# Optimization experiments

Hardware: AMD Instinct MI355X
Metric: run time of the kernel (lower is better)

## Reference

```python
import jax, jax.numpy as jnp
import numpy as np

B, S, E, H = 2, 2048, 1024, 16
DH = E // H  # 64


def setup_inputs() -> dict:
    key = jax.random.key(0)
    ks = jax.random.split(key, 5)
    scale = 1.0 / np.sqrt(E)
    x = jax.random.normal(ks[0], (B, S, E), dtype=jnp.float32)
    # stacked per-head kqv Linear weights: out = x @ Wkqv[h] + bkqv[h], producing (k, q, v) chunks
    Wkqv = jax.random.normal(ks[1], (H, E, 3 * DH), dtype=jnp.float32) * scale
    bkqv = jax.random.normal(ks[2], (H, 3 * DH), dtype=jnp.float32) * scale
    Wo = jax.random.normal(ks[3], (E, E), dtype=jnp.float32) * scale
    bo = jax.random.normal(ks[4], (E,), dtype=jnp.float32) * scale
    return {"x": x, "Wkqv": Wkqv, "bkqv": bkqv, "Wo": Wo, "bo": bo}


def reference(x, Wkqv, bkqv, Wo, bo):
    b, s, e = x.shape
    h, _, f = Wkqv.shape
    dh = f // 3
    # per-head projection, fused over heads: [b, h, s, 3*dh]
    kqv = jnp.einsum('bse,hef->bhsf', x, Wkqv) + bkqv[None, :, None, :]
    # chunk order in the original is k, q, v
    k, q, v = jnp.split(kqv, 3, axis=-1)
    scores = jnp.einsum('bhqd,bhkd->bhqk', q, k) / jnp.sqrt(jnp.asarray(dh, x.dtype))
    causal = jnp.tril(jnp.ones((s, s), dtype=bool))  # slice of the tril buffer
    scores = jnp.where(causal[None, None], scores, -jnp.inf)
    weights = jax.nn.softmax(scores, axis=-1)
    sa = jnp.einsum('bhqk,bhkd->bhqd', weights, v)
    # concat heads along feature dim (head order preserved)
    sa = sa.transpose(0, 2, 1, 3).reshape(b, s, h * dh)
    return sa @ Wo + bo
```

## Files before the change

### kernel.cpp

```cpp
#include <hip/hip_runtime.h>
#include <hip/hip_bf16.h>

typedef __attribute__((ext_vector_type(8))) short bf16x8;
typedef __attribute__((ext_vector_type(4))) float f32x4;
typedef __attribute__((ext_vector_type(2))) unsigned u32x2;
typedef __attribute__((ext_vector_type(4))) unsigned u32x4;
typedef unsigned short u16;

#define NEG_INF (-__builtin_inff())

__device__ __forceinline__ void gload16(const void* g, void* l) {
  __builtin_amdgcn_global_load_lds(
      (const __attribute__((address_space(1))) void*)g,
      (__attribute__((address_space(3))) void*)l, 16, 0, 0);
}

__device__ __forceinline__ u16 f2b(float f) {
  union { float f; unsigned u; } v;
  v.f = f;
  unsigned r = v.u + 0x7fff + ((v.u >> 16) & 1);
  return (u16)(r >> 16);
}

__device__ __forceinline__ unsigned cvt_pk_bf16(float a, float b) {
  unsigned r;
  asm("v_cvt_pk_bf16_f32 %0, %1, %2" : "=v"(r) : "v"(a), "v"(b));
  return r;
}

__global__ __launch_bounds__(256) void prep_kernel(
    const float* __restrict__ x, u16* __restrict__ xb,
    const float* __restrict__ Wkqv, u16* __restrict__ WkqvT,
    const float* __restrict__ Wo, u16* __restrict__ WoT) {
  __shared__ u16 t[32][33];
  const int bid = blockIdx.x;
  const int tid = threadIdx.x;
  if (bid < 4096) {
    const int i = bid * 256 + tid;
    float4 v = ((const float4*)x)[i];
    ushort2 a = {f2b(v.x), f2b(v.y)}, b = {f2b(v.z), f2b(v.w)};
    ((ushort2*)xb)[i * 2] = a;
    ((ushort2*)xb)[i * 2 + 1] = b;
    return;
  }
  const int tx = tid & 31, ty = tid >> 5;
  const float* src;
  u16* dst;
  int R, C, bx_, by;
  if (bid < 7168) {
    const int tt = bid - 4096;
    const int bz = tt / 192, rem = tt % 192;
    by = rem / 6; bx_ = rem % 6; R = 1024; C = 192;
    src = Wkqv + (size_t)bz * R * C;
    dst = WkqvT + (size_t)bz * R * C;
  } else {
    const int tt = bid - 7168;
    by = tt >> 5; bx_ = tt & 31; R = 1024; C = 1024;
    src = Wo; dst = WoT;
  }
  const int c0 = bx_ * 32, r0 = by * 32;
  for (int i = ty; i < 32; i += 8)
    t[i][tx] = f2b(src[(size_t)(r0 + i) * C + c0 + tx]);
  __syncthreads();
  for (int i = ty; i < 32; i += 8)
    dst[(size_t)(c0 + i) * R + r0 + tx] = t[tx][i];
}

__device__ __forceinline__ void gemm_mainloop_128(
    const __hip_bfloat16* __restrict__ A, const __hip_bfloat16* __restrict__ Bt,
    int K, int m0, int n0, f32x4 acc[4][4], char* AsB, char* BsB) {
  const int tid = threadIdx.x;
  const int wave = tid >> 6, lane = tid & 63;
  const int lhi = lane >> 4, llo = lane & 15;
  const int wr = wave >> 1, wc = wave & 1;
  f32x4 z = {0.f, 0.f, 0.f, 0.f};
#pragma unroll
  for (int i = 0; i < 4; i++)
#pragma unroll
    for (int j = 0; j < 4; j++) acc[i][j] = z;

#define GSTAGE(c, kk)                                                          \
  {                                                                            \
    char* AsW = AsB + (c)*8192;                                                \
    char* BsW = BsB + (c)*8192;                                                \
    _Pragma("unroll") for (int i = 0; i < 2; i++) {                            \
      int cb = i * 256 + wave * 64;                                            \
      int cq = cb + lane;                                                      \
      gload16(A + ((size_t)(m0 + (cq >> 2)) * K + (kk) + (cq & 3) * 8),        \
              AsW + cb * 16);                                                  \
      gload16(Bt + ((size_t)(n0 + (cq >> 2)) * K + (kk) + (cq & 3) * 8),       \
              BsW + cb * 16);                                                  \
    }                                                                          \
  }

  GSTAGE(0, 0);
  int cur = 0;
  const int nk = K >> 5;
  for (int t = 0; t < nk; t++) {
    if (t + 1 < nk) {
      GSTAGE(cur ^ 1, (t + 1) * 32);
      asm volatile("s_waitcnt vmcnt(4)" ::: "memory");
    } else {
      asm volatile("s_waitcnt vmcnt(0)" ::: "memory");
    }
    __builtin_amdgcn_s_barrier();
    __builtin_amdgcn_sched_barrier(0);

    const char* Ar = AsB + cur * 8192;
    const char* Br = BsB + cur * 8192;
    bf16x8 a[4], b[4];
#pragma unroll
    for (int m4 = 0; m4 < 4; m4++)
      a[m4] = *(const bf16x8*)(Ar + (wr * 64 + m4 * 16 + llo) * 64 + lhi * 16);
#pragma unroll
    for (int n4 = 0; n4 < 4; n4++)
      b[n4] = *(const bf16x8*)(Br + (wc * 64 + n4 * 16 + llo) * 64 + lhi * 16);
#pragma unroll
    for (int m4 = 0; m4 < 4; m4++)
#pragma unroll
      for (int n4 = 0; n4 < 4; n4++)
        acc[m4][n4] =
            __builtin_amdgcn_mfma_f32_16x16x32_bf16(a[m4], b[n4], acc[m4][n4], 0, 0, 0);
    __builtin_amdgcn_sched_barrier(0);
    __builtin_amdgcn_s_barrier();
    cur ^= 1;
  }
#undef GSTAGE
}

__device__ __forceinline__ void gemm_mainloop_64x128(
    const __hip_bfloat16* __restrict__ A, const __hip_bfloat16* __restrict__ Bt,
    int K, int m0, int n0, f32x4 acc[2][4], char* AsB, char* BsB) {
  const int tid = threadIdx.x;
  const int wave = tid >> 6, lane = tid & 63;
  const int lhi = lane >> 4, llo = lane & 15;
  const int wr = wave >> 1, wc = wave & 1;
  f32x4 z = {0.f, 0.f, 0.f, 0.f};
#pragma unroll
  for (int i = 0; i < 2; i++)
#pragma unroll
    for (int j = 0; j < 4; j++) acc[i][j] = z;

#define GSTAGE64(c, kk)                                                        \
  {                                                                            \
    char* AsW = AsB + (c)*4096;                                                \
    char* BsW = BsB + (c)*8192;                                                \
    gload16(A + ((size_t)(m0 + (tid >> 2)) * K + (kk) + (tid & 3) * 8),        \
            AsW + (wave * 64) * 16);                                           \
    _Pragma("unroll") for (int i = 0; i < 2; i++) {                            \
      int cb = i * 256 + wave * 64;                                            \
      int cq = cb + lane;                                                      \
      gload16(Bt + ((size_t)(n0 + (cq >> 2)) * K + (kk) + (cq & 3) * 8),       \
              BsW + cb * 16);                                                  \
    }                                                                          \
  }

  GSTAGE64(0, 0);
  int cur = 0;
  const int nk = K >> 5;
  for (int t = 0; t < nk; t++) {
    if (t + 1 < nk) {
      GSTAGE64(cur ^ 1, (t + 1) * 32);
      asm volatile("s_waitcnt vmcnt(3)" ::: "memory");
    } else {
      asm volatile("s_waitcnt vmcnt(0)" ::: "memory");
    }
    __builtin_amdgcn_s_barrier();
    __builtin_amdgcn_sched_barrier(0);

    const char* Ar = AsB + cur * 4096;
    const char* Br = BsB + cur * 8192;
    bf16x8 a[2], b[4];
#pragma unroll
    for (int m2 = 0; m2 < 2; m2++)
      a[m2] = *(const bf16x8*)(Ar + (wr * 32 + m2 * 16 + llo) * 64 + lhi * 16);
#pragma unroll
    for (int n4 = 0; n4 < 4; n4++)
      b[n4] = *(const bf16x8*)(Br + (wc * 64 + n4 * 16 + llo) * 64 + lhi * 16);
#pragma unroll
    for (int m2 = 0; m2 < 2; m2++)
#pragma unroll
      for (int n4 = 0; n4 < 4; n4++)
        acc[m2][n4] =
            __builtin_amdgcn_mfma_f32_16x16x32_bf16(a[m2], b[n4], acc[m2][n4], 0, 0, 0);
    __builtin_amdgcn_sched_barrier(0);
    __builtin_amdgcn_s_barrier();
    cur ^= 1;
  }
#undef GSTAGE64
}

__global__ __launch_bounds__(256) void kqv_gemm(
    const __hip_bfloat16* __restrict__ x, const __hip_bfloat16* __restrict__ WT,
    const float* __restrict__ bkqv, __hip_bfloat16* __restrict__ Qb,
    __hip_bfloat16* __restrict__ Kb, __hip_bfloat16* __restrict__ Vt) {
  __shared__ __align__(16) char As[16384];
  __shared__ __align__(16) char Bs[16384];
  const int m0 = blockIdx.y * 128, n0 = blockIdx.x * 128;
  f32x4 acc[4][4];
  gemm_mainloop_128(x, WT, 1024, m0, n0, acc, As, Bs);

  const int tid = threadIdx.x, wave = tid >> 6, lane = tid & 63;
  const int lhi = lane >> 4, llo = lane & 15;
  const int wr = wave >> 1, wc = wave & 1;
#pragma unroll
  for (int m4 = 0; m4 < 4; m4++)
#pragma unroll
    for (int n4 = 0; n4 < 4; n4++)
#pragma unroll
      for (int r = 0; r < 4; r++) {
        int mg = m0 + wr * 64 + m4 * 16 + lhi * 4 + r;
        int ng = n0 + wc * 64 + n4 * 16 + llo;
        int b = mg >> 11, s = mg & 2047;
        int h = ng / 192, f = ng % 192;
        float v = acc[m4][n4][r] + bkqv[h * 192 + f];
        int chunk = f >> 6, d = f & 63;
        size_t bh = (size_t)(b * 16 + h);
        if (chunk == 0)
          Kb[(bh * 2048 + s) * 64 + d] = __float2bfloat16(v);
        else if (chunk == 1)
          Qb[(bh * 2048 + s) * 64 + d] = __float2bfloat16(v * 0.180336880f);
        else
          Vt[(bh * 64 + d) * 2048 + s] = __float2bfloat16(v);
      }
}

__global__ __launch_bounds__(256) void attn_kernel(
    const __hip_bfloat16* __restrict__ Qb, const __hip_bfloat16* __restrict__ Kb,
    const __hip_bfloat16* __restrict__ Vt, __hip_bfloat16* __restrict__ SA) {
  __shared__ __align__(16) char lds[32768];
  const int orig = blockIdx.x;
  const int bh = (orig & 7) * 4 + ((orig >> 3) & 3);
  const int qt = 31 - (orig >> 5);
  const int nt = qt + 1;
  const int b = bh >> 4, h = bh & 15;
  const int tid = threadIdx.x, wave = tid >> 6, lane = tid & 63;
  const int lhi = lane >> 4, llo = lane & 15;
  const int lhi4 = lhi * 4;

  const __hip_bfloat16* qp =
      Qb + ((size_t)bh * 2048 + qt * 64 + wave * 16 + llo) * 64 + lhi * 8;
  bf16x8 q0 = *(const bf16x8*)qp, q1 = *(const bf16x8*)(qp + 32);

  const char* Kg = (const char*)(Kb + (size_t)bh * 2048 * 64);
  const char* Vg = (const char*)(Vt + (size_t)bh * 64 * 2048);

  f32x4 z = {0.f, 0.f, 0.f, 0.f};
  f32x4 o[4];
  float m_s = NEG_INF, l_s = 0.f;
#pragma unroll
  for (int i = 0; i < 4; i++) o[i] = z;
  const int qg = qt * 64 + wave * 16 + llo;
  const int qg0 = qt * 64 + wave * 16 + lhi4;

#define STAGE(c, k0)                                                          \
  {                                                                           \
    char* KsW = lds + (c)*8192;                                               \
    char* VsW = lds + 16384 + (c)*8192;                                       \
    _Pragma("unroll") for (int i = 0; i < 2; i++) {                           \
      int ch = i * 256 + tid;                                                 \
      int soff = (ch * 16) ^ (((ch >> 3) & 7) << 4);                          \
      gload16(Kg + (size_t)(k0)*128 + soff, KsW + (i * 256 + wave * 64) * 16);\
      int dd = ch >> 3, c8 = ch & 7;                                          \
      int boff = (c8 * 16) ^ ((dd & 7) << 4);                                 \
      gload16(Vg + (size_t)dd * 4096 + (size_t)(k0)*2 + boff,                 \
              VsW + (i * 256 + wave * 64) * 16);                              \
    }                                                                         \
  }

  STAGE(0, 0);
  int cur = 0;

  for (int T = 0; T < nt; T++) {
    if (T + 1 < nt) {
      STAGE(cur ^ 1, (T + 1) * 64);
      asm volatile("s_waitcnt vmcnt(4)" ::: "memory");
    } else {
      asm volatile("s_waitcnt vmcnt(0)" ::: "memory");
    }
    __builtin_amdgcn_s_barrier();
    __builtin_amdgcn_sched_barrier(0);

    const int k0 = T * 64;
    const bool masked = (T == nt - 1);
    const char* KsB = lds + cur * 8192;
    const char* VsB = lds + 16384 + cur * 8192;

    f32x4 s[4] = {z, z, z, z};
#pragma unroll
    for (int j = 0; j < 4; j++) {
      const int row = j * 16 + llo;
      const int rx = (row & 7) << 4;
      bf16x8 bk0 = *(const bf16x8*)(KsB + ((row * 128 + lhi * 16) ^ rx));
      bf16x8 bk1 = *(const bf16x8*)(KsB + ((row * 128 + 64 + lhi * 16) ^ rx));
      s[j] = __builtin_amdgcn_mfma_f32_16x16x32_bf16(bk0, q0, s[j], 0, 0, 0);
      s[j] = __builtin_amdgcn_mfma_f32_16x16x32_bf16(bk1, q1, s[j], 0, 0, 0);
    }

    if (masked) {
#pragma unroll
      for (int j = 0; j < 4; j++)
#pragma unroll
        for (int r = 0; r < 4; r++)
          if (k0 + j * 16 + lhi4 + r > qg) s[j][r] = NEG_INF;
    }
    float pmax = s[0][0];
#pragma unroll
    for (int j = 0; j < 4; j++)
#pragma unroll
      for (int r = 0; r < 4; r++) pmax = fmaxf(pmax, s[j][r]);
    {
      union { float f; unsigned u; } pu;
      pu.f = pmax;
      u32x2 sp = __builtin_amdgcn_permlane32_swap(pu.u, pu.u, false, false);
      float m1 = fmaxf(__uint_as_float(sp.x), __uint_as_float(sp.y));
      union { float f; unsigned u; } mu;
      mu.f = m1;
      u32x2 tp = __builtin_amdgcn_permlane16_swap(mu.u, mu.u, false, false);
      pmax = fmaxf(__uint_as_float(tp.x), __uint_as_float(tp.y));
    }
    if (!__all(pmax - m_s <= 5.0f)) {
      const float mn = fmaxf(m_s, pmax);
      const float sc = __builtin_exp2f(m_s - mn);
      m_s = mn;
      l_s *= sc;
#pragma unroll
      for (int r = 0; r < 4; r++) {
        const float scr = __shfl(sc, lhi4 + r);
#pragma unroll
        for (int n4 = 0; n4 < 4; n4++) o[n4][r] *= scr;
      }
    }

    unsigned pk[4][2];
    float ps = 0.f;
#pragma unroll
    for (int j = 0; j < 4; j++) {
      float p0 = __builtin_exp2f(s[j][0] - m_s);
      float p1 = __builtin_exp2f(s[j][1] - m_s);
      float p2 = __builtin_exp2f(s[j][2] - m_s);
      float p3 = __builtin_exp2f(s[j][3] - m_s);
      ps += (p0 + p1) + (p2 + p3);
      pk[j][0] = cvt_pk_bf16(p0, p1);
      pk[j][1] = cvt_pk_bf16(p2, p3);
    }
    l_s += ps;

    u32x4 a0w, a1w;
#pragma unroll
    for (int u = 0; u < 2; u++) {
      u32x2 sp = __builtin_amdgcn_permlane32_swap(pk[0][u], pk[1][u], false, false);
      u32x2 tp = __builtin_amdgcn_permlane16_swap(sp.x, sp.y, false, false);
      a0w[u] = tp.x;
      a0w[u + 2] = tp.y;
    }
#pragma unroll
    for (int u = 0; u < 2; u++) {
      u32x2 sp = __builtin_amdgcn_permlane32_swap(pk[2][u], pk[3][u], false, false);
      u32x2 tp = __builtin_amdgcn_permlane16_swap(sp.x, sp.y, false, false);
      a1w[u] = tp.x;
      a1w[u + 2] = tp.y;
    }
    bf16x8 ap0 = __builtin_bit_cast(bf16x8, a0w);
    bf16x8 ap1 = __builtin_bit_cast(bf16x8, a1w);

#pragma unroll
    for (int n4 = 0; n4 < 4; n4++) {
      const int d = n4 * 16 + llo;
      const int dx = (d & 7) << 4;
      bf16x8 bv0 = *(const bf16x8*)(VsB + ((d * 128 + lhi * 16) ^ dx));
      bf16x8 bv1 = *(const bf16x8*)(VsB + ((d * 128 + 64 + lhi * 16) ^ dx));
      o[n4] = __builtin_amdgcn_mfma_f32_16x16x32_bf16(ap0, bv0, o[n4], 0, 0, 0);
      o[n4] = __builtin_amdgcn_mfma_f32_16x16x32_bf16(ap1, bv1, o[n4], 0, 0, 0);
    }
    __builtin_amdgcn_sched_barrier(0);
    __builtin_amdgcn_s_barrier();
    cur ^= 1;
  }

  {
    union { float f; unsigned u; } lu;
    lu.f = l_s;
    u32x2 sp = __builtin_amdgcn_permlane32_swap(lu.u, lu.u, false, false);
    float l1 = __uint_as_float(sp.x) + __uint_as_float(sp.y);
    union { float f; unsigned u; } l2u;
    l2u.f = l1;
    u32x2 tp = __builtin_amdgcn_permlane16_swap(l2u.u, l2u.u, false, false);
    const float l = __uint_as_float(tp.x) + __uint_as_float(tp.y);
    const float inv = 1.f / l;
#pragma unroll
    for (int r = 0; r < 4; r++) {
      const float invr = __shfl(inv, lhi4 + r);
      const size_t ob = ((size_t)b * 2048 + qg0 + r) * 1024 + h * 64;
#pragma unroll
      for (int n4 = 0; n4 < 4; n4++)
        SA[ob + n4 * 16 + llo] = __float2bfloat16(o[n4][r] * invr);
    }
  }
#undef STAGE
}

__global__ __launch_bounds__(256) void out_gemm(
    const __hip_bfloat16* __restrict__ SA, const __hip_bfloat16* __restrict__ WoT,
    const float* __restrict__ bo, float* __restrict__ out) {
  __shared__ __align__(16) char As[8192];
  __shared__ __align__(16) char Bs[16384];
  const int m0 = blockIdx.y * 64, n0 = blockIdx.x * 128;
  f32x4 acc[2][4];
  gemm_mainloop_64x128(SA, WoT, 1024, m0, n0, acc, As, Bs);

  const int tid = threadIdx.x, wave = tid >> 6, lane = tid & 63;
  const int lhi = lane >> 4, llo = lane & 15;
  const int wr = wave >> 1, wc = wave & 1;
#pragma unroll
  for (int m2 = 0; m2 < 2; m2++)
#pragma unroll
    for (int n4 = 0; n4 < 4; n4++)
#pragma unroll
      for (int r = 0; r < 4; r++) {
        int mg = m0 + wr * 32 + m2 * 16 + lhi * 4 + r;
        int ng = n0 + wc * 64 + n4 * 16 + llo;
        out[(size_t)mg * 1024 + ng] = acc[m2][n4][r] + bo[ng];
      }
}

extern "C" void kernel_launch(void* const* d_in, const int* in_sizes, int n_in,
                              void* d_out, int out_size, void* d_ws, size_t ws_size,
                              hipStream_t stream) {
  const float* x = (const float*)d_in[0];
  const float* Wkqv = (const float*)d_in[1];
  const float* bkqv = (const float*)d_in[2];
  const float* Wo = (const float*)d_in[3];
  const float* bo = (const float*)d_in[4];
  float* out = (float*)d_out;

  char* w = (char*)d_ws;
  __hip_bfloat16* WkqvT = (__hip_bfloat16*)(w);
  __hip_bfloat16* WoT = (__hip_bfloat16*)(w + 6291456);
  __hip_bfloat16* Qb = (__hip_bfloat16*)(w + 8388608);
  __hip_bfloat16* Kb = (__hip_bfloat16*)(w + 16777216);
  __hip_bfloat16* Vt = (__hip_bfloat16*)(w + 25165824);
  __hip_bfloat16* SAb = (__hip_bfloat16*)(w + 33554432);
  __hip_bfloat16* xb = (__hip_bfloat16*)(w + 41943040);

  prep_kernel<<<8192, 256, 0, stream>>>(x, (u16*)xb, Wkqv, (u16*)WkqvT,
                                        Wo, (u16*)WoT);
  kqv_gemm<<<dim3(24, 32), 256, 0, stream>>>(xb, WkqvT, bkqv, Qb, Kb, Vt);
  attn_kernel<<<1024, 256, 0, stream>>>(Qb, Kb, Vt, SAb);
  out_gemm<<<dim3(8, 64), 256, 0, stream>>>(SAb, WoT, bo, out);
}
```

Baseline: 118.0 us.

## Enlarge attention query tile to 128 rows with 8 waves sharing K/V loads

Attention blocks now cover 128 query rows with 512 threads (8 waves) instead of 64 rows with 4 waves, halving the grid. Each K/V tile staged into LDS is reused by twice as many waves, and each thread issues one load per tensor per stage instead of two. Waves whose rows lie entirely before the current key tile skip the compute, using per-wave causal bounds. The tradeoff is fewer blocks and more idle waves on the diagonal tiles, plus possible occupancy changes from the larger block size.

```diff
diff --git a/kernel.cpp b/kernel.cpp
--- a/kernel.cpp
+++ b/kernel.cpp
@@ -225,21 +225,23 @@
       }
 }
 
-__global__ __launch_bounds__(256) void attn_kernel(
+__global__ __launch_bounds__(512) void attn_kernel(
     const __hip_bfloat16* __restrict__ Qb, const __hip_bfloat16* __restrict__ Kb,
     const __hip_bfloat16* __restrict__ Vt, __hip_bfloat16* __restrict__ SA) {
   __shared__ __align__(16) char lds[32768];
   const int orig = blockIdx.x;
-  const int bh = (orig & 7) * 4 + ((orig >> 3) & 3);
-  const int qt = 31 - (orig >> 5);
-  const int nt = qt + 1;
+  const int xcd = orig & 7, j = orig >> 3;
+  const int bh = xcd * 4 + (j & 3);
+  const int t = 15 - (j >> 2);
+  const int qoff = t * 128;
+  const int nt = 2 * t + 2;
   const int b = bh >> 4, h = bh & 15;
   const int tid = threadIdx.x, wave = tid >> 6, lane = tid & 63;
   const int lhi = lane >> 4, llo = lane & 15;
   const int lhi4 = lhi * 4;
 
   const __hip_bfloat16* qp =
-      Qb + ((size_t)bh * 2048 + qt * 64 + wave * 16 + llo) * 64 + lhi * 8;
+      Qb + ((size_t)bh * 2048 + qoff + wave * 16 + llo) * 64 + lhi * 8;
   bf16x8 q0 = *(const bf16x8*)qp, q1 = *(const bf16x8*)(qp + 32);
 
   const char* Kg = (const char*)(Kb + (size_t)bh * 2048 * 64);
@@ -250,22 +252,20 @@
   float m_s = NEG_INF, l_s = 0.f;
 #pragma unroll
   for (int i = 0; i < 4; i++) o[i] = z;
-  const int qg = qt * 64 + wave * 16 + llo;
-  const int qg0 = qt * 64 + wave * 16 + lhi4;
+  const int qg = qoff + wave * 16 + llo;
+  const int qg0 = qoff + wave * 16 + lhi4;
+  const int wave_rmax = qoff + wave * 16 + 15;
 
 #define STAGE(c, k0)                                                          \
   {                                                                           \
     char* KsW = lds + (c)*8192;                                               \
     char* VsW = lds + 16384 + (c)*8192;                                       \
-    _Pragma("unroll") for (int i = 0; i < 2; i++) {                           \
-      int ch = i * 256 + tid;                                                 \
-      int soff = (ch * 16) ^ (((ch >> 3) & 7) << 4);                          \
-      gload16(Kg + (size_t)(k0)*128 + soff, KsW + (i * 256 + wave * 64) * 16);\
-      int dd = ch >> 3, c8 = ch & 7;                                          \
-      int boff = (c8 * 16) ^ ((dd & 7) << 4);                                 \
-      gload16(Vg + (size_t)dd * 4096 + (size_t)(k0)*2 + boff,                 \
-              VsW + (i * 256 + wave * 64) * 16);                              \
-    }                                                                         \
+    const int ch = tid;                                                       \
+    int soff = (ch * 16) ^ (((ch >> 3) & 7) << 4);                            \
+    gload16(Kg + (size_t)(k0)*128 + soff, KsW + wave * 1024);                 \
+    int dd = ch >> 3, c8 = ch & 7;                                            \
+    int boff = (c8 * 16) ^ ((dd & 7) << 4);                                   \
+    gload16(Vg + (size_t)dd * 4096 + (size_t)(k0)*2 + boff, VsW + wave * 1024);\
   }
 
   STAGE(0, 0);
@@ -274,7 +274,7 @@
   for (int T = 0; T < nt; T++) {
     if (T + 1 < nt) {
       STAGE(cur ^ 1, (T + 1) * 64);
-      asm volatile("s_waitcnt vmcnt(4)" ::: "memory");
+      asm volatile("s_waitcnt vmcnt(2)" ::: "memory");
     } else {
       asm volatile("s_waitcnt vmcnt(0)" ::: "memory");
     }
@@ -282,96 +282,98 @@
     __builtin_amdgcn_sched_barrier(0);
 
     const int k0 = T * 64;
-    const bool masked = (T == nt - 1);
-    const char* KsB = lds + cur * 8192;
-    const char* VsB = lds + 16384 + cur * 8192;
-
-    f32x4 s[4] = {z, z, z, z};
-#pragma unroll
-    for (int j = 0; j < 4; j++) {
-      const int row = j * 16 + llo;
-      const int rx = (row & 7) << 4;
-      bf16x8 bk0 = *(const bf16x8*)(KsB + ((row * 128 + lhi * 16) ^ rx));
-      bf16x8 bk1 = *(const bf16x8*)(KsB + ((row * 128 + 64 + lhi * 16) ^ rx));
-      s[j] = __builtin_amdgcn_mfma_f32_16x16x32_bf16(bk0, q0, s[j], 0, 0, 0);
-      s[j] = __builtin_amdgcn_mfma_f32_16x16x32_bf16(bk1, q1, s[j], 0, 0, 0);
-    }
-
-    if (masked) {
-#pragma unroll
-      for (int j = 0; j < 4; j++)
-#pragma unroll
-        for (int r = 0; r < 4; r++)
-          if (k0 + j * 16 + lhi4 + r > qg) s[j][r] = NEG_INF;
-    }
-    float pmax = s[0][0];
-#pragma unroll
-    for (int j = 0; j < 4; j++)
-#pragma unroll
-      for (int r = 0; r < 4; r++) pmax = fmaxf(pmax, s[j][r]);
-    {
-      union { float f; unsigned u; } pu;
-      pu.f = pmax;
-      u32x2 sp = __builtin_amdgcn_permlane32_swap(pu.u, pu.u, false, false);
-      float m1 = fmaxf(__uint_as_float(sp.x), __uint_as_float(sp.y));
-      union { float f; unsigned u; } mu;
-      mu.f = m1;
-      u32x2 tp = __builtin_amdgcn_permlane16_swap(mu.u, mu.u, false, false);
-      pmax = fmaxf(__uint_as_float(tp.x), __uint_as_float(tp.y));
-    }
-    if (!__all(pmax - m_s <= 5.0f)) {
-      const float mn = fmaxf(m_s, pmax);
-      const float sc = __builtin_exp2f(m_s - mn);
-      m_s = mn;
-      l_s *= sc;
-#pragma unroll
-      for (int r = 0; r < 4; r++) {
-        const float scr = __shfl(sc, lhi4 + r);
-#pragma unroll
-        for (int n4 = 0; n4 < 4; n4++) o[n4][r] *= scr;
-      }
-    }
-
-    unsigned pk[4][2];
-    float ps = 0.f;
-#pragma unroll
-    for (int j = 0; j < 4; j++) {
-      float p0 = __builtin_exp2f(s[j][0] - m_s);
-      float p1 = __builtin_exp2f(s[j][1] - m_s);
-      float p2 = __builtin_exp2f(s[j][2] - m_s);
-      float p3 = __builtin_exp2f(s[j][3] - m_s);
-      ps += (p0 + p1) + (p2 + p3);
-      pk[j][0] = cvt_pk_bf16(p0, p1);
-      pk[j][1] = cvt_pk_bf16(p2, p3);
-    }
-    l_s += ps;
-
-    u32x4 a0w, a1w;
-#pragma unroll
-    for (int u = 0; u < 2; u++) {
-      u32x2 sp = __builtin_amdgcn_permlane32_swap(pk[0][u], pk[1][u], false, false);
-      u32x2 tp = __builtin_amdgcn_permlane16_swap(sp.x, sp.y, false, false);
-      a0w[u] = tp.x;
-      a0w[u + 2] = tp.y;
-    }
-#pragma unroll
-    for (int u = 0; u < 2; u++) {
-      u32x2 sp = __builtin_amdgcn_permlane32_swap(pk[2][u], pk[3][u], false, false);
-      u32x2 tp = __builtin_amdgcn_permlane16_swap(sp.x, sp.y, false, false);
-      a1w[u] = tp.x;
-      a1w[u + 2] = tp.y;
-    }
-    bf16x8 ap0 = __builtin_bit_cast(bf16x8, a0w);
-    bf16x8 ap1 = __builtin_bit_cast(bf16x8, a1w);
-
-#pragma unroll
-    for (int n4 = 0; n4 < 4; n4++) {
-      const int d = n4 * 16 + llo;
-      const int dx = (d & 7) << 4;
-      bf16x8 bv0 = *(const bf16x8*)(VsB + ((d * 128 + lhi * 16) ^ dx));
-      bf16x8 bv1 = *(const bf16x8*)(VsB + ((d * 128 + 64 + lhi * 16) ^ dx));
-      o[n4] = __builtin_amdgcn_mfma_f32_16x16x32_bf16(ap0, bv0, o[n4], 0, 0, 0);
-      o[n4] = __builtin_amdgcn_mfma_f32_16x16x32_bf16(ap1, bv1, o[n4], 0, 0, 0);
+    if (k0 <= wave_rmax) {
+      const bool masked = (k0 + 63 > wave_rmax - 15);
+      const char* KsB = lds + cur * 8192;
+      const char* VsB = lds + 16384 + cur * 8192;
+
+      f32x4 s[4] = {z, z, z, z};
+#pragma unroll
+      for (int jj = 0; jj < 4; jj++) {
+        const int row = jj * 16 + llo;
+        const int rx = (row & 7) << 4;
+        bf16x8 bk0 = *(const bf16x8*)(KsB + ((row * 128 + lhi * 16) ^ rx));
+        bf16x8 bk1 = *(const bf16x8*)(KsB + ((row * 128 + 64 + lhi * 16) ^ rx));
+        s[jj] = __builtin_amdgcn_mfma_f32_16x16x32_bf16(bk0, q0, s[jj], 0, 0, 0);
+        s[jj] = __builtin_amdgcn_mfma_f32_16x16x32_bf16(bk1, q1, s[jj], 0, 0, 0);
+      }
+
+      if (masked) {
+#pragma unroll
+        for (int jj = 0; jj < 4; jj++)
+#pragma unroll
+          for (int r = 0; r < 4; r++)
+            if (k0 + jj * 16 + lhi4 + r > qg) s[jj][r] = NEG_INF;
+      }
+      float pmax = s[0][0];
+#pragma unroll
+      for (int jj = 0; jj < 4; jj++)
+#pragma unroll
+        for (int r = 0; r < 4; r++) pmax = fmaxf(pmax, s[jj][r]);
+      {
+        union { float f; unsigned u; } pu;
+        pu.f = pmax;
+        u32x2 sp = __builtin_amdgcn_permlane32_swap(pu.u, pu.u, false, false);
+        float m1 = fmaxf(__uint_as_float(sp.x), __uint_as_float(sp.y));
+        union { float f; unsigned u; } mu;
+        mu.f = m1;
+        u32x2 tp = __builtin_amdgcn_permlane16_swap(mu.u, mu.u, false, false);
+        pmax = fmaxf(__uint_as_float(tp.x), __uint_as_float(tp.y));
+      }
+      if (!__all(pmax - m_s <= 5.0f)) {
+        const float mn = fmaxf(m_s, pmax);
+        const float sc = __builtin_exp2f(m_s - mn);
+        m_s = mn;
+        l_s *= sc;
+#pragma unroll
+        for (int r = 0; r < 4; r++) {
+          const float scr = __shfl(sc, lhi4 + r);
+#pragma unroll
+          for (int n4 = 0; n4 < 4; n4++) o[n4][r] *= scr;
+        }
+      }
+
+      unsigned pk[4][2];
+      float ps = 0.f;
+#pragma unroll
+      for (int jj = 0; jj < 4; jj++) {
+        float p0 = __builtin_exp2f(s[jj][0] - m_s);
+        float p1 = __builtin_exp2f(s[jj][1] - m_s);
+        float p2 = __builtin_exp2f(s[jj][2] - m_s);
+        float p3 = __builtin_exp2f(s[jj][3] - m_s);
+        ps += (p0 + p1) + (p2 + p3);
+        pk[jj][0] = cvt_pk_bf16(p0, p1);
+        pk[jj][1] = cvt_pk_bf16(p2, p3);
+      }
+      l_s += ps;
+
+      u32x4 a0w, a1w;
+#pragma unroll
+      for (int u = 0; u < 2; u++) {
+        u32x2 sp = __builtin_amdgcn_permlane32_swap(pk[0][u], pk[1][u], false, false);
+        u32x2 tp = __builtin_amdgcn_permlane16_swap(sp.x, sp.y, false, false);
+        a0w[u] = tp.x;
+        a0w[u + 2] = tp.y;
+      }
+#pragma unroll
+      for (int u = 0; u < 2; u++) {
+        u32x2 sp = __builtin_amdgcn_permlane32_swap(pk[2][u], pk[3][u], false, false);
+        u32x2 tp = __builtin_amdgcn_permlane16_swap(sp.x, sp.y, false, false);
+        a1w[u] = tp.x;
+        a1w[u + 2] = tp.y;
+      }
+      bf16x8 ap0 = __builtin_bit_cast(bf16x8, a0w);
+      bf16x8 ap1 = __builtin_bit_cast(bf16x8, a1w);
+
+#pragma unroll
+      for (int n4 = 0; n4 < 4; n4++) {
+        const int d = n4 * 16 + llo;
+        const int dx = (d & 7) << 4;
+        bf16x8 bv0 = *(const bf16x8*)(VsB + ((d * 128 + lhi * 16) ^ dx));
+        bf16x8 bv1 = *(const bf16x8*)(VsB + ((d * 128 + 64 + lhi * 16) ^ dx));
+        o[n4] = __builtin_amdgcn_mfma_f32_16x16x32_bf16(ap0, bv0, o[n4], 0, 0, 0);
+        o[n4] = __builtin_amdgcn_mfma_f32_16x16x32_bf16(ap1, bv1, o[n4], 0, 0, 0);
+      }
     }
     __builtin_amdgcn_sched_barrier(0);
     __builtin_amdgcn_s_barrier();
@@ -446,6 +448,6 @@
   prep_kernel<<<8192, 256, 0, stream>>>(x, (u16*)xb, Wkqv, (u16*)WkqvT,
                                         Wo, (u16*)WoT);
   kqv_gemm<<<dim3(24, 32), 256, 0, stream>>>(xb, WkqvT, bkqv, Qb, Kb, Vt);
-  attn_kernel<<<1024, 256, 0, stream>>>(Qb, Kb, Vt, SAb);
+  attn_kernel<<<512, 512, 0, stream>>>(Qb, Kb, Vt, SAb);
   out_gemm<<<dim3(8, 64), 256, 0, stream>>>(SAb, WoT, bo, out);
 }
```

Measured after the change: 119.7 us. No clear change (+1.5%).
